# Performance work log

Hardware: AMD Instinct MI355X
Metric: run time of the kernel (lower is better)

## Reference

```python
import jax, jax.numpy as jnp
import numpy as np

B, D, H, DOUT, E, K = 8192, 1024, 4096, 1024, 8, 2


def setup_inputs() -> dict:
    key = jax.random.key(0)
    ks = jax.random.split(key, 7)
    s_d = 1.0 / np.sqrt(D)
    s_h = 1.0 / np.sqrt(H)
    return {
        "x": jax.random.normal(ks[0], (B, D), jnp.float32),
        "Wg": jax.random.uniform(ks[1], (D, E), jnp.float32, -s_d, s_d),
        "bg": jax.random.uniform(ks[2], (E,), jnp.float32, -s_d, s_d),
        "W1": jax.random.uniform(ks[3], (E, D, H), jnp.float32, -s_d, s_d),
        "b1": jax.random.uniform(ks[4], (E, H), jnp.float32, -s_d, s_d),
        "W2": jax.random.uniform(ks[5], (E, H, DOUT), jnp.float32, -s_h, s_h),
        "b2": jax.random.uniform(ks[6], (E, DOUT), jnp.float32, -s_h, s_h),
    }


def reference(x, Wg, bg, W1, b1, W2, b2):
    # gating
    gate_probs = jax.nn.softmax(x @ Wg + bg, axis=-1)          # [B, E]
    top_k_probs, top_k_idx = jax.lax.top_k(gate_probs, K)       # [B, K]
    top_k_probs = top_k_probs / jnp.sum(top_k_probs, axis=-1, keepdims=True)

    # dense all-expert compute (faithful to torch.stack over experts)
    h = jax.nn.gelu(jnp.einsum('bd,edh->beh', x, W1) + b1, approximate=False)  # [B, E, H]
    expert_outputs = jnp.einsum('beh,eho->beo', h, W2) + b2                    # [B, E, DOUT]

    # gather selected experts and combine
    sel = jnp.take_along_axis(expert_outputs, top_k_idx[:, :, None], axis=1)   # [B, K, DOUT]
    output = jnp.sum(sel * top_k_probs[:, :, None], axis=1)                    # [B, DOUT]

    # load-balancing aux loss (as written in the original)
    expert_usage = jnp.mean(gate_probs, axis=0)                # [E]
    uniform = jnp.full_like(expert_usage, 1.0 / E)
    aux_loss = jnp.sum(expert_usage * jnp.log(uniform) - jnp.log(expert_usage) * uniform)
    return output, aux_loss
```

## Files before the change

### kernel.cpp

```cpp
#include <hip/hip_runtime.h>
#include <hip/hip_bf16.h>
#include <hip/hip_fp16.h>

#define B_    8192
#define D_    1024
#define H_    4096
#define DOUT_ 1024
#define E_    8
#define MAXR  17408

typedef float    f32x4 __attribute__((ext_vector_type(4)));
typedef _Float16 f16x8 __attribute__((ext_vector_type(8)));
typedef unsigned short u16;
typedef u16      u16x8 __attribute__((ext_vector_type(8)));
typedef u16      u16x4 __attribute__((ext_vector_type(4)));
typedef unsigned int u32;

__device__ __forceinline__ u16 f2h_bits(float f) {
  _Float16 h = (_Float16)f;
  return __builtin_bit_cast(u16, h);
}

__device__ __forceinline__ float gelu_f(float v) {
  float z = 0.7978845608028654f * (v + 0.044715f * v * v * v);
  float ez = __expf(2.f * z);
  float th = 1.f - 2.f / (ez + 1.f);
  return 0.5f * v * (1.f + th);
}

#define OFF_TOPI 512
#define OFF_TOPW (OFF_TOPI + 65536)
#define OFF_ATOK (OFF_TOPW + 65536)
#define OFF_WSL  (OFF_ATOK + 69632)
#define OFF_XG   524288
#define OFF_W1T  (OFF_XG + 35651584)
#define OFF_W2T  OFF_XG
#define OFF_HB   (OFF_W1T + 67108864)

__global__ void k_zero_out(float* __restrict__ out) {
  size_t i = (size_t)(blockIdx.x * 256 + threadIdx.x) * 4;
  *(f32x4*)&out[i] = (f32x4){0.f, 0.f, 0.f, 0.f};
}

__global__ void k_init(int* __restrict__ atok, float* __restrict__ wslot,
                       int* __restrict__ meta) {
  int i = blockIdx.x * 256 + threadIdx.x;
  if (i < MAXR) { atok[i] = 0; wslot[i] = 0.f; }
  if (blockIdx.x == 0 && threadIdx.x < 64) meta[threadIdx.x] = 0;
}

__global__ __launch_bounds__(256) void k_gate(
    const float* __restrict__ x, const float* __restrict__ Wg,
    const float* __restrict__ bg, int* __restrict__ counts,
    float* __restrict__ usage, int* __restrict__ topi, float* __restrict__ topw) {
  __shared__ float su[E_];
  if (threadIdx.x < E_) su[threadIdx.x] = 0.f;
  __syncthreads();
  const int lane = threadIdx.x & 63;
  const int b = blockIdx.x * 4 + (threadIdx.x >> 6);
  float p[E_] = {0.f,0.f,0.f,0.f,0.f,0.f,0.f,0.f};
  #pragma unroll
  for (int j = 0; j < 4; ++j) {
    int d = j * 256 + lane * 4;
    float4 xv = *(const float4*)&x[(size_t)b * D_ + d];
    const float* wr = &Wg[(size_t)d * E_];
    #pragma unroll
    for (int c = 0; c < 4; ++c) {
      float xc = reinterpret_cast<const float*>(&xv)[c];
      #pragma unroll
      for (int e = 0; e < E_; ++e) p[e] += xc * wr[c * E_ + e];
    }
  }
  #pragma unroll
  for (int off = 32; off >= 1; off >>= 1)
    #pragma unroll
    for (int e = 0; e < E_; ++e) p[e] += __shfl_xor(p[e], off, 64);
  float mx = -1e30f;
  #pragma unroll
  for (int e = 0; e < E_; ++e) { p[e] += bg[e]; mx = fmaxf(mx, p[e]); }
  int i0 = 0; float l0 = p[0];
  #pragma unroll
  for (int e = 1; e < E_; ++e) if (p[e] > l0) { l0 = p[e]; i0 = e; }
  int i1 = -1; float l1 = -1e30f;
  #pragma unroll
  for (int e = 0; e < E_; ++e) if (e != i0 && p[e] > l1) { l1 = p[e]; i1 = e; }
  float s = 0.f;
  #pragma unroll
  for (int e = 0; e < E_; ++e) { p[e] = expf(p[e] - mx); s += p[e]; }
  float inv = 1.f / s;
  if (lane == 0) {
    float e0 = expf(l0 - mx), e1 = expf(l1 - mx);
    float wsum = e0 + e1;
    topi[b * 2] = i0; topi[b * 2 + 1] = i1;
    topw[b * 2] = e0 / wsum; topw[b * 2 + 1] = e1 / wsum;
    atomicAdd(&counts[i0], 1);
    atomicAdd(&counts[i1], 1);
    #pragma unroll
    for (int e = 0; e < E_; ++e) atomicAdd(&su[e], p[e] * inv);
  }
  __syncthreads();
  if (threadIdx.x < E_) atomicAdd(&usage[threadIdx.x], su[threadIdx.x]);
}

__global__ void k_scan_aux(const int* __restrict__ counts, int* __restrict__ offsets,
                           const float* __restrict__ usage, float* __restrict__ auxp) {
  if (threadIdx.x == 0) {
    int off = 0;
    for (int e = 0; e < E_; ++e) { offsets[e] = off; off += (counts[e] + 127) & ~127; }
    offsets[E_] = off;
    float aux = 0.f;
    const float lu = logf(1.0f / (float)E_);
    for (int e = 0; e < E_; ++e) {
      float u = usage[e] * (1.0f / (float)B_);
      aux += u * lu - logf(u) * (1.0f / (float)E_);
    }
    *auxp = aux;
  }
}

__global__ void k_scatter(const int* __restrict__ topi, const float* __restrict__ topw,
                          const int* __restrict__ offsets, int* __restrict__ cursors,
                          int* __restrict__ atok, float* __restrict__ wslot) {
  int b = blockIdx.x * 256 + threadIdx.x;
  if (b >= B_) return;
  #pragma unroll
  for (int k = 0; k < 2; ++k) {
    int e = topi[b * 2 + k];
    int pos = atomicAdd(&cursors[e], 1);
    int slot = offsets[e] + pos;
    atok[slot] = b;
    wslot[slot] = topw[b * 2 + k];
  }
}

__global__ __launch_bounds__(256) void k_gather(const float* __restrict__ x,
                                                const int* __restrict__ atok,
                                                u16* __restrict__ Xg) {
  int slot = blockIdx.x;
  int tok = atok[slot];
  int c = threadIdx.x * 4;
  float4 v = *(const float4*)&x[(size_t)tok * D_ + c];
  const float* vf = reinterpret_cast<const float*>(&v);
  u16x4 o;
  o.x = f2h_bits(vf[0]); o.y = f2h_bits(vf[1]);
  o.z = f2h_bits(vf[2]); o.w = f2h_bits(vf[3]);
  *(u16x4*)&Xg[(size_t)slot * D_ + c] = o;
}

__global__ __launch_bounds__(256) void k_cvt_t(const float* __restrict__ src,
                                               u16* __restrict__ dst, int K, int N) {
  const int e = blockIdx.z;
  const int kt = blockIdx.x * 64;
  const int nt = blockIdx.y * 64;
  __shared__ u16 t[64][68];
  const float* s = src + (size_t)e * K * N;
  u16* d = dst + (size_t)e * N * K;
  const int tr = threadIdx.x >> 4;
  const int tc = threadIdx.x & 15;
  #pragma unroll
  for (int i = 0; i < 4; ++i) {
    int k = tr + i * 16;
    float4 v = *(const float4*)&s[(size_t)(kt + k) * N + nt + tc * 4];
    t[k][tc*4+0] = f2h_bits(v.x); t[k][tc*4+1] = f2h_bits(v.y);
    t[k][tc*4+2] = f2h_bits(v.z); t[k][tc*4+3] = f2h_bits(v.w);
  }
  __syncthreads();
  #pragma unroll
  for (int i = 0; i < 4; ++i) {
    int n = tr + i * 16;
    u16x4 o;
    o.x = t[tc*4+0][n]; o.y = t[tc*4+1][n];
    o.z = t[tc*4+2][n]; o.w = t[tc*4+3][n];
    *(u16x4*)&d[(size_t)(nt + n) * K + kt + tc * 4] = o;
  }
}

#define GLDS(g, l) __builtin_amdgcn_global_load_lds( \
    (const u32 __attribute__((address_space(1)))*)(g), \
    (u32 __attribute__((address_space(3)))*)(l), 16, 0, 0)

#define VMWAIT(N) asm volatile("s_waitcnt vmcnt(" #N ")" ::: "memory")
#define BARRIER() do { __builtin_amdgcn_s_barrier(); \
                       asm volatile("" ::: "memory"); } while (0)

#define NXT(x) ((x) == 24576 ? 0 : (x) + 12288)

#define STG3(LDK, kt, sb) do { \
  const int r_ = lane >> 2; \
  const int sc_ = ((lane & 3) ^ ((r_ ^ (r_ >> 2)) & 3)) * 8; \
  { \
    int rw = wid * 16 + r_; \
    GLDS(Ap + (size_t)rw * (LDK) + (kt) * 32 + sc_, SM + (sb) + wid * 512); \
  } \
  _Pragma("unroll") \
  for (int j = 0; j < 2; ++j) { \
    int seg = wid * 2 + j; \
    GLDS(Bp + (size_t)(seg * 16 + r_) * (LDK) + (kt) * 32 + sc_, \
         SM + (sb) + 4096 + seg * 512); \
  } } while (0)

#define RD_FR(rb_) do { \
  const int r15_ = lane & 15; \
  const int co_ = (((lane >> 4) ^ ((r15_ ^ (r15_ >> 2)) & 3)) * 8); \
  _Pragma("unroll") \
  for (int mi = 0; mi < 4; ++mi) \
    af[mi] = *(const f16x8*)&SM[(rb_) + (wr * 64 + mi * 16 + r15_) * 32 + co_]; \
  _Pragma("unroll") \
  for (int n = 0; n < 4; ++n) \
    bf[n] = *(const f16x8*)&SM[(rb_) + 4096 + (wc * 64 + n * 16 + r15_) * 32 + co_]; \
} while (0)

#define MM16() do { \
  __builtin_amdgcn_s_setprio(1); \
  _Pragma("unroll") \
  for (int mi = 0; mi < 4; ++mi) \
    _Pragma("unroll") \
    for (int n = 0; n < 4; ++n) \
      acc[mi][n] = __builtin_amdgcn_mfma_f32_16x16x32_f16(af[mi], bf[n], acc[mi][n], 0, 0, 0); \
  __builtin_amdgcn_s_setprio(0); \
} while (0)

#define KLOOP(LDK, NT) do { \
  int rb = 0, wb = 24576; \
  STG3(LDK, 0, 0); \
  STG3(LDK, 1, 12288); \
  VMWAIT(3); \
  BARRIER(); \
  for (int t = 0; t < (NT); ++t) { \
    RD_FR(rb); \
    if (t + 2 < (NT)) STG3(LDK, t + 2, wb); \
    BARRIER(); \
    MM16(); \
    if (t + 2 < (NT)) VMWAIT(3); \
    else if (t + 1 < (NT)) VMWAIT(0); \
    BARRIER(); \
    rb = NXT(rb); wb = NXT(wb); \
  } \
} while (0)

__global__ __launch_bounds__(512, 4) void k_gemm1(
    const u16* __restrict__ Xg, const u16* __restrict__ W1t,
    const float* __restrict__ b1, const int* __restrict__ offsets,
    u16* __restrict__ Hb) {
  const int L = blockIdx.x;
  const int mtile = L >> 4;
  const int nt = L & 15;
  const int row0 = mtile * 128;
  if (row0 >= offsets[E_]) return;
  int e = 0;
  #pragma unroll
  for (int i = 1; i < E_; ++i) e = (row0 >= offsets[i]) ? i : e;
  const int n0 = nt * 256;
  const int tid = threadIdx.x, lane = tid & 63, wid = tid >> 6;
  const int wr = wid >> 2, wc = wid & 3;
  __shared__ __align__(16) u16 SM[36864];
  f32x4 acc[4][4] = {};
  f16x8 af[4], bf[4];
  const u16* Ap = Xg + (size_t)row0 * D_;
  const u16* Bp = W1t + (size_t)e * H_ * D_ + (size_t)n0 * D_;

  KLOOP(D_, 32);

  const int rhi = (lane >> 4) * 4, cix = lane & 15;
  float bv[4];
  #pragma unroll
  for (int n = 0; n < 4; ++n) bv[n] = b1[e * H_ + n0 + wc * 64 + n * 16 + cix];
  #pragma unroll
  for (int r = 0; r < 2; ++r) {
    if (wr == r) {
      #pragma unroll
      for (int m = 0; m < 4; ++m)
        #pragma unroll
        for (int n = 0; n < 4; ++n)
          #pragma unroll
          for (int j = 0; j < 4; ++j)
            SM[(m * 16 + rhi + j) * 264 + wc * 64 + n * 16 + cix] =
                f2h_bits(gelu_f(acc[m][n][j] + bv[n]));
    }
    __syncthreads();
    {
      const int rl = tid >> 3, co = (tid & 7) * 32;
      u16* dst = &Hb[(size_t)(row0 + r * 64 + rl) * H_ + n0 + co];
      const u16* srcp = &SM[rl * 264 + co];
      #pragma unroll
      for (int qq = 0; qq < 4; ++qq)
        *(u16x8*)(dst + qq * 8) = *(const u16x8*)(srcp + qq * 8);
    }
    __syncthreads();
  }
}

__global__ __launch_bounds__(512, 4) void k_gemm2(
    const u16* __restrict__ Hb, const u16* __restrict__ W2t,
    const float* __restrict__ b2, const int* __restrict__ offsets,
    const int* __restrict__ atok, const float* __restrict__ wslot,
    float* __restrict__ out) {
  const int L = blockIdx.x;
  const int mtile = L >> 2;
  const int nt = L & 3;
  const int row0 = mtile * 128;
  if (row0 >= offsets[E_]) return;
  int e = 0;
  #pragma unroll
  for (int i = 1; i < E_; ++i) e = (row0 >= offsets[i]) ? i : e;
  const int n0 = nt * 256;
  const int kbase = blockIdx.y * 2048;
  const int tid = threadIdx.x, lane = tid & 63, wid = tid >> 6;
  const int wr = wid >> 2, wc = wid & 3;
  __shared__ __align__(16) u16 SM[36864];
  f32x4 acc[4][4] = {};
  f16x8 af[4], bf[4];
  const u16* Ap = Hb + (size_t)row0 * H_ + kbase;
  const u16* Bp = W2t + (size_t)e * DOUT_ * H_ + (size_t)n0 * H_ + kbase;

  KLOOP(H_, 64);

  const int rhi = (lane >> 4) * 4, cix = lane & 15;
  const int first = (kbase == 0);
  float bv[4];
  #pragma unroll
  for (int n = 0; n < 4; ++n) bv[n] = b2[e * DOUT_ + n0 + wc * 64 + n * 16 + cix];
  #pragma unroll
  for (int m = 0; m < 4; ++m) {
    #pragma unroll
    for (int j = 0; j < 4; ++j) {
      int slot = row0 + wr * 64 + m * 16 + rhi + j;
      float w = wslot[slot];
      if (w == 0.f) continue;
      int tok = atok[slot];
      float* orow = out + (size_t)tok * DOUT_ + n0;
      #pragma unroll
      for (int n = 0; n < 4; ++n) {
        int lc = wc * 64 + n * 16 + cix;
        float v = first ? w * (acc[m][n][j] + bv[n]) : w * acc[m][n][j];
        atomicAdd(&orow[lc], v);
      }
    }
  }
}

extern "C" void kernel_launch(void* const* d_in, const int* in_sizes, int n_in,
                              void* d_out, int out_size, void* d_ws, size_t ws_size,
                              hipStream_t stream) {
  const float* x  = (const float*)d_in[0];
  const float* Wg = (const float*)d_in[1];
  const float* bg = (const float*)d_in[2];
  const float* W1 = (const float*)d_in[3];
  const float* b1 = (const float*)d_in[4];
  const float* W2 = (const float*)d_in[5];
  const float* b2 = (const float*)d_in[6];
  float* out = (float*)d_out;

  char* ws = (char*)d_ws;
  int*   counts  = (int*)(ws + 0);
  int*   cursors = (int*)(ws + 32);
  int*   offsets = (int*)(ws + 64);
  float* usage   = (float*)(ws + 128);
  int*   topi    = (int*)(ws + OFF_TOPI);
  float* topw    = (float*)(ws + OFF_TOPW);
  int*   atok    = (int*)(ws + OFF_ATOK);
  float* wslot   = (float*)(ws + OFF_WSL);
  u16*   Xg      = (u16*)(ws + OFF_XG);
  u16*   W1t     = (u16*)(ws + OFF_W1T);
  u16*   W2t     = (u16*)(ws + OFF_W2T);
  u16*   Hb      = (u16*)(ws + OFF_HB);

  k_zero_out<<<B_ * DOUT_ / 1024, 256, 0, stream>>>(out);
  k_init<<<(MAXR + 255) / 256, 256, 0, stream>>>(atok, wslot, (int*)ws);
  k_gate<<<B_ / 4, 256, 0, stream>>>(x, Wg, bg, counts, usage, topi, topw);
  k_scan_aux<<<1, 64, 0, stream>>>(counts, offsets, usage, out + (size_t)B_ * DOUT_);
  k_scatter<<<B_ / 256, 256, 0, stream>>>(topi, topw, offsets, cursors, atok, wslot);
  k_gather<<<MAXR, 256, 0, stream>>>(x, atok, Xg);
  k_cvt_t<<<dim3(D_ / 64, H_ / 64, E_), 256, 0, stream>>>(W1, W1t, D_, H_);
  k_gemm1<<<(MAXR / 128) * 16, 512, 0, stream>>>(Xg, W1t, b1, offsets, Hb);
  k_cvt_t<<<dim3(H_ / 64, DOUT_ / 64, E_), 256, 0, stream>>>(W2, W2t, H_, DOUT_);
  k_gemm2<<<dim3((MAXR / 128) * 4, 2), 512, 0, stream>>>(Hb, W2t, b2, offsets, atok, wslot, out);
}
```

Baseline: 818.4 us.

## Replace atomic scatter-add epilogue with fp16 expert outputs and combine kernel

GEMM2 no longer splits K across two blocks or atomically adds weighted results into the output. Each block now computes the full K range, adds the bias and writes an fp16 per-slot expert output through shared memory. A new combine kernel reads each token's two slots and writes the weighted sum directly, so the output zeroing kernel is no longer needed. This removes float atomics and the zero fill, but halves GEMM2 grid parallelism and adds an fp16 intermediate round trip, which costs some precision.

Result: faster. 800.6 us (-2.2%).

```diff
diff --git a/kernel.cpp b/kernel.cpp
--- a/kernel.cpp
+++ b/kernel.cpp
@@ -20,6 +20,9 @@
   _Float16 h = (_Float16)f;
   return __builtin_bit_cast(u16, h);
 }
+__device__ __forceinline__ float h2f(u16 b) {
+  return (float)__builtin_bit_cast(_Float16, b);
+}
 
 __device__ __forceinline__ float gelu_f(float v) {
   float z = 0.7978845608028654f * (v + 0.044715f * v * v * v);
@@ -32,15 +35,12 @@
 #define OFF_TOPW (OFF_TOPI + 65536)
 #define OFF_ATOK (OFF_TOPW + 65536)
 #define OFF_WSL  (OFF_ATOK + 69632)
+#define OFF_SLOT (OFF_WSL + 69632)
 #define OFF_XG   524288
 #define OFF_W1T  (OFF_XG + 35651584)
 #define OFF_W2T  OFF_XG
+#define OFF_Y    (OFF_XG + 67108864)
 #define OFF_HB   (OFF_W1T + 67108864)
-
-__global__ void k_zero_out(float* __restrict__ out) {
-  size_t i = (size_t)(blockIdx.x * 256 + threadIdx.x) * 4;
-  *(f32x4*)&out[i] = (f32x4){0.f, 0.f, 0.f, 0.f};
-}
 
 __global__ void k_init(int* __restrict__ atok, float* __restrict__ wslot,
                        int* __restrict__ meta) {
@@ -120,7 +120,8 @@
 
 __global__ void k_scatter(const int* __restrict__ topi, const float* __restrict__ topw,
                           const int* __restrict__ offsets, int* __restrict__ cursors,
-                          int* __restrict__ atok, float* __restrict__ wslot) {
+                          int* __restrict__ atok, float* __restrict__ wslot,
+                          int* __restrict__ slot_of) {
   int b = blockIdx.x * 256 + threadIdx.x;
   if (b >= B_) return;
   #pragma unroll
@@ -130,6 +131,7 @@
     int slot = offsets[e] + pos;
     atok[slot] = b;
     wslot[slot] = topw[b * 2 + k];
+    slot_of[b * 2 + k] = slot;
   }
 }
 
@@ -293,8 +295,7 @@
 __global__ __launch_bounds__(512, 4) void k_gemm2(
     const u16* __restrict__ Hb, const u16* __restrict__ W2t,
     const float* __restrict__ b2, const int* __restrict__ offsets,
-    const int* __restrict__ atok, const float* __restrict__ wslot,
-    float* __restrict__ out) {
+    u16* __restrict__ Y) {
   const int L = blockIdx.x;
   const int mtile = L >> 2;
   const int nt = L & 3;
@@ -304,39 +305,60 @@
   #pragma unroll
   for (int i = 1; i < E_; ++i) e = (row0 >= offsets[i]) ? i : e;
   const int n0 = nt * 256;
-  const int kbase = blockIdx.y * 2048;
   const int tid = threadIdx.x, lane = tid & 63, wid = tid >> 6;
   const int wr = wid >> 2, wc = wid & 3;
   __shared__ __align__(16) u16 SM[36864];
   f32x4 acc[4][4] = {};
   f16x8 af[4], bf[4];
-  const u16* Ap = Hb + (size_t)row0 * H_ + kbase;
-  const u16* Bp = W2t + (size_t)e * DOUT_ * H_ + (size_t)n0 * H_ + kbase;
-
-  KLOOP(H_, 64);
+  const u16* Ap = Hb + (size_t)row0 * H_;
+  const u16* Bp = W2t + (size_t)e * DOUT_ * H_ + (size_t)n0 * H_;
+
+  KLOOP(H_, 128);
 
   const int rhi = (lane >> 4) * 4, cix = lane & 15;
-  const int first = (kbase == 0);
   float bv[4];
   #pragma unroll
   for (int n = 0; n < 4; ++n) bv[n] = b2[e * DOUT_ + n0 + wc * 64 + n * 16 + cix];
   #pragma unroll
-  for (int m = 0; m < 4; ++m) {
-    #pragma unroll
-    for (int j = 0; j < 4; ++j) {
-      int slot = row0 + wr * 64 + m * 16 + rhi + j;
-      float w = wslot[slot];
-      if (w == 0.f) continue;
-      int tok = atok[slot];
-      float* orow = out + (size_t)tok * DOUT_ + n0;
+  for (int r = 0; r < 2; ++r) {
+    if (wr == r) {
       #pragma unroll
-      for (int n = 0; n < 4; ++n) {
-        int lc = wc * 64 + n * 16 + cix;
-        float v = first ? w * (acc[m][n][j] + bv[n]) : w * acc[m][n][j];
-        atomicAdd(&orow[lc], v);
-      }
-    }
-  }
+      for (int m = 0; m < 4; ++m)
+        #pragma unroll
+        for (int n = 0; n < 4; ++n)
+          #pragma unroll
+          for (int j = 0; j < 4; ++j)
+            SM[(m * 16 + rhi + j) * 264 + wc * 64 + n * 16 + cix] =
+                f2h_bits(acc[m][n][j] + bv[n]);
+    }
+    __syncthreads();
+    {
+      const int rl = tid >> 3, co = (tid & 7) * 32;
+      u16* dst = &Y[(size_t)(row0 + r * 64 + rl) * DOUT_ + n0 + co];
+      const u16* srcp = &SM[rl * 264 + co];
+      #pragma unroll
+      for (int qq = 0; qq < 4; ++qq)
+        *(u16x8*)(dst + qq * 8) = *(const u16x8*)(srcp + qq * 8);
+    }
+    __syncthreads();
+  }
+}
+
+__global__ __launch_bounds__(256) void k_combine(
+    const u16* __restrict__ Y, const float* __restrict__ topw,
+    const int* __restrict__ slot_of, float* __restrict__ out) {
+  const int b = blockIdx.x;
+  const int c = threadIdx.x * 4;
+  const int s0 = slot_of[b * 2], s1 = slot_of[b * 2 + 1];
+  const float w0 = topw[b * 2], w1 = topw[b * 2 + 1];
+  u16x4 y0 = *(const u16x4*)&Y[(size_t)s0 * DOUT_ + c];
+  u16x4 y1 = *(const u16x4*)&Y[(size_t)s1 * DOUT_ + c];
+  float4 o;
+  o.x = w0 * h2f(y0.x) + w1 * h2f(y1.x);
+  o.y = w0 * h2f(y0.y) + w1 * h2f(y1.y);
+  o.z = w0 * h2f(y0.z) + w1 * h2f(y1.z);
+  o.w = w0 * h2f(y0.w) + w1 * h2f(y1.w);
+  *(float4*)&out[(size_t)b * DOUT_ + c] = o;
 }
 
 extern "C" void kernel_launch(void* const* d_in, const int* in_sizes, int n_in,
@@ -360,19 +382,21 @@
   float* topw    = (float*)(ws + OFF_TOPW);
   int*   atok    = (int*)(ws + OFF_ATOK);
   float* wslot   = (float*)(ws + OFF_WSL);
+  int*   slot_of = (int*)(ws + OFF_SLOT);
   u16*   Xg      = (u16*)(ws + OFF_XG);
   u16*   W1t     = (u16*)(ws + OFF_W1T);
   u16*   W2t     = (u16*)(ws + OFF_W2T);
+  u16*   Y       = (u16*)(ws + OFF_Y);
   u16*   Hb      = (u16*)(ws + OFF_HB);
 
-  k_zero_out<<<B_ * DOUT_ / 1024, 256, 0, stream>>>(out);
   k_init<<<(MAXR + 255) / 256, 256, 0, stream>>>(atok, wslot, (int*)ws);
   k_gate<<<B_ / 4, 256, 0, stream>>>(x, Wg, bg, counts, usage, topi, topw);
   k_scan_aux<<<1, 64, 0, stream>>>(counts, offsets, usage, out + (size_t)B_ * DOUT_);
-  k_scatter<<<B_ / 256, 256, 0, stream>>>(topi, topw, offsets, cursors, atok, wslot);
+  k_scatter<<<B_ / 256, 256, 0, stream>>>(topi, topw, offsets, cursors, atok, wslot, slot_of);
   k_gather<<<MAXR, 256, 0, stream>>>(x, atok, Xg);
   k_cvt_t<<<dim3(D_ / 64, H_ / 64, E_), 256, 0, stream>>>(W1, W1t, D_, H_);
   k_gemm1<<<(MAXR / 128) * 16, 512, 0, stream>>>(Xg, W1t, b1, offsets, Hb);
   k_cvt_t<<<dim3(H_ / 64, DOUT_ / 64, E_), 256, 0, stream>>>(W2, W2t, H_, DOUT_);
-  k_gemm2<<<dim3((MAXR / 128) * 4, 2), 512, 0, stream>>>(Hb, W2t, b2, offsets, atok, wslot, out);
-}
+  k_gemm2<<<(MAXR / 128) * 4, 512, 0, stream>>>(Hb, W2t, b2, offsets, Y);
+  k_combine<<<B_, 256, 0, stream>>>(Y, topw, slot_of, out);
+}
```
